# Performance work log

Hardware: AMD Instinct MI355X
Metric: run time of the kernel (lower is better)

The kernel has to match this reference:

```python
import jax, jax.numpy as jnp
import numpy as np

B, L, D = 2, 2048, 1024
H, DH = 16, 64            # heads, dim_head; inner_dim = H*DH = 1024
SCALE = DH ** -0.5


def setup_inputs() -> dict:
    key = jax.random.key(0)
    ks = jax.random.split(key, 7)
    s = 0.02
    return {
        "x": jax.random.normal(ks[0], (B, L, D), dtype=jnp.float32),
        "attention_mask": jnp.zeros((B * H, L, L), dtype=jnp.float32),
        "Wq": jax.random.normal(ks[1], (H * DH, D), dtype=jnp.float32) * s,
        "Wk": jax.random.normal(ks[2], (H * DH, D), dtype=jnp.float32) * s,
        "Wv": jax.random.normal(ks[3], (H * DH, D), dtype=jnp.float32) * s,
        "Wo": jax.random.normal(ks[4], (D, H * DH), dtype=jnp.float32) * s,
        "bo": jnp.zeros((D,), dtype=jnp.float32),
    }


def _split_heads(t):
    # [B, L, H*DH] -> [(B*H), L, DH]
    b, l, _ = t.shape
    return t.reshape(b, l, H, DH).transpose(0, 2, 1, 3).reshape(b * H, l, DH)


def reference(x, attention_mask, Wq, Wk, Wv, Wo, bo):
    # Self-attention: encoder_hidden_states = hidden_states
    q = _split_heads(jnp.einsum('bld,ed->ble', x, Wq))  # [(B*H), L, DH]
    k = _split_heads(jnp.einsum('bld,ed->ble', x, Wk))
    v = _split_heads(jnp.einsum('bld,ed->ble', x, Wv))
    # baddbmm: mask + scale * q @ k^T  -> [(B*H), L, L]
    scores = attention_mask + SCALE * jnp.einsum('nqd,nkd->nqk', q, k)
    probs = jax.nn.softmax(scores, axis=-1)
    hidden = jnp.einsum('nqk,nkd->nqd', probs, v)       # [(B*H), L, DH]
    hidden = hidden.reshape(B, H, L, DH).transpose(0, 2, 1, 3).reshape(B, L, H * DH)
    return jnp.einsum('ble,de->bld', hidden, Wo) + bo   # out projection (dropout=0)
```

## Files before the change

### kernel.cpp

```cpp
#include <hip/hip_runtime.h>


typedef __attribute__((ext_vector_type(8))) short short8;
typedef __attribute__((ext_vector_type(8))) __bf16 bf16x8;
typedef __attribute__((ext_vector_type(4))) float f32x4;

#define GLDS16(gp, lp)                                                         \
  __builtin_amdgcn_global_load_lds(                                            \
      (const __attribute__((address_space(1))) void*)(gp),                     \
      (__attribute__((address_space(3))) void*)(lp), 16, 0, 0)

__device__ __forceinline__ unsigned short f2bf(float f) {
  unsigned u = __builtin_bit_cast(unsigned, f);
  u += 0x7fffu + ((u >> 16) & 1u);
  return (unsigned short)(u >> 16);
}

__global__ __launch_bounds__(256) void convert_all(
    const float* __restrict__ x, const float* __restrict__ wq,
    const float* __restrict__ wk, const float* __restrict__ wv,
    const float* __restrict__ wo, unsigned short* __restrict__ xb,
    unsigned short* __restrict__ wqkv, unsigned short* __restrict__ wob) {
  const int X4 = (2 * 2048 * 1024) / 4;
  const int W4 = (1024 * 1024) / 4;
  const int total = X4 + 4 * W4;
  for (int i = blockIdx.x * 256 + threadIdx.x; i < total;
       i += gridDim.x * 256) {
    const float* src; unsigned short* dst; int off;
    if (i < X4)               { src = x;  dst = xb;                   off = i; }
    else if (i < X4 + W4)     { src = wq; dst = wqkv;                 off = i - X4; }
    else if (i < X4 + 2 * W4) { src = wk; dst = wqkv + 1024 * 1024;   off = i - X4 - W4; }
    else if (i < X4 + 3 * W4) { src = wv; dst = wqkv + 2 * 1024 * 1024; off = i - X4 - 2 * W4; }
    else                      { src = wo; dst = wob;                  off = i - X4 - 3 * W4; }
    float4 v = ((const float4*)src)[off];
    uint2 o;
    o.x = (unsigned)f2bf(v.x) | ((unsigned)f2bf(v.y) << 16);
    o.y = (unsigned)f2bf(v.z) | ((unsigned)f2bf(v.w) << 16);
    ((uint2*)dst)[off] = o;
  }
}

template <int MODE>
__global__ __launch_bounds__(256, 2) void gemm_bt(
    const unsigned short* __restrict__ A, const unsigned short* __restrict__ Bw,
    unsigned short* __restrict__ o_q, unsigned short* __restrict__ o_k,
    unsigned short* __restrict__ o_vT, const float* __restrict__ bias,
    float* __restrict__ o_f) {
  constexpr int K = 1024;
  __shared__ unsigned short As[128 * 32];
  __shared__ unsigned short Bs[128 * 32];
  const int t = threadIdx.x;
  const int w = t >> 6;
  const int lane = t & 63;
  const int g = lane >> 4;
  const int q16 = lane & 15;
  const int wm = w >> 1, wn = w & 1;
  const int bn0 = blockIdx.x * 128, bm0 = blockIdx.y * 128;
  const int arow = t >> 2;
  const int acol = (t & 3) * 8;

  f32x4 acc[4][4];
  const f32x4 z4 = {0.f, 0.f, 0.f, 0.f};
#pragma unroll
  for (int i = 0; i < 4; ++i)
#pragma unroll
    for (int j = 0; j < 4; ++j) acc[i][j] = z4;

  for (int k0 = 0; k0 < K; k0 += 32) {
#pragma unroll
    for (int c = 0; c < 2; ++c) {
      GLDS16(A + (size_t)(bm0 + c * 64 + arow) * K + k0 + acol,
             As + c * 2048 + w * 512);
      GLDS16(Bw + (size_t)(bn0 + c * 64 + arow) * K + k0 + acol,
             Bs + c * 2048 + w * 512);
    }
    __syncthreads();
    bf16x8 af[4], bf[4];
#pragma unroll
    for (int i = 0; i < 4; ++i)
      af[i] = *(const bf16x8*)(As + (wm * 64 + i * 16 + q16) * 32 + g * 8);
#pragma unroll
    for (int j = 0; j < 4; ++j)
      bf[j] = *(const bf16x8*)(Bs + (wn * 64 + j * 16 + q16) * 32 + g * 8);
#pragma unroll
    for (int i = 0; i < 4; ++i)
#pragma unroll
      for (int j = 0; j < 4; ++j)
        acc[i][j] =
            __builtin_amdgcn_mfma_f32_16x16x32_bf16(af[i], bf[j], acc[i][j], 0, 0, 0);
    __syncthreads();
  }

  if constexpr (MODE == 0) {
    const int which = bn0 >> 10;
#pragma unroll
    for (int i = 0; i < 4; ++i)
#pragma unroll
      for (int j = 0; j < 4; ++j)
#pragma unroll
        for (int r = 0; r < 4; ++r) {
          const int m = bm0 + wm * 64 + i * 16 + g * 4 + r;
          const int n = (bn0 & 1023) + wn * 64 + j * 16 + q16;
          const float v = acc[i][j][r];
          const int bb = m >> 11, lp = m & 2047;
          const int h = n >> 6, d = n & 63;
          const int bh = bb * 16 + h;
          if (which == 0)
            o_q[((size_t)bh * 2048 + lp) * 64 + d] = f2bf(v * 0.125f);
          else if (which == 1)
            o_k[((size_t)bh * 2048 + lp) * 64 + d] = f2bf(v);
          else
            o_vT[((size_t)bh * 64 + d) * 2048 + lp] = f2bf(v);
        }
  } else {
#pragma unroll
    for (int i = 0; i < 4; ++i)
#pragma unroll
      for (int j = 0; j < 4; ++j)
#pragma unroll
        for (int r = 0; r < 4; ++r) {
          const int m = bm0 + wm * 64 + i * 16 + g * 4 + r;
          const int n = bn0 + wn * 64 + j * 16 + q16;
          o_f[(size_t)m * 1024 + n] = acc[i][j][r] + bias[n];
        }
  }
}

__global__ __launch_bounds__(256, 3) void attn_kernel(
    const unsigned short* __restrict__ kb, const unsigned short* __restrict__ qb,
    const unsigned short* __restrict__ vT, const float* __restrict__ mask,
    unsigned short* __restrict__ hb) {
  __shared__ float Mst[3 * 2048];
  __shared__ unsigned short Kst[2 * 2048];
  __shared__ unsigned short Vst[2 * 2048];
  __shared__ unsigned short Plds[4][16][40];
  const int orig = blockIdx.x;
  const int bid = (orig & 7) * 128 + (orig >> 3);
  const int bh = bid >> 5, qt = bid & 31;
  const int t = threadIdx.x, w = t >> 6, lane = t & 63;
  const int g = lane >> 4, q16 = lane & 15;
  const int qrow0 = qt * 64;
  const int qrow = qrow0 + w * 16;

  const unsigned short* qptr = qb + ((size_t)bh * 2048 + qrow + q16) * 64 + g * 8;
  bf16x8 qf0 = *(const bf16x8*)(qptr);
  bf16x8 qf1 = *(const bf16x8*)(qptr + 32);

  f32x4 O[4];
  const f32x4 z4 = {0.f, 0.f, 0.f, 0.f};
#pragma unroll
  for (int dt = 0; dt < 4; ++dt) O[dt] = z4;
  float mrun = -1e30f, lsum = 0.f;

  const float* mbase = mask + ((size_t)bh * 2048 + qrow0) * 2048;
  const int fA = (w * 2 + 0) * 64 + lane;
  const int fB = (w * 2 + 1) * 64 + lane;
  const int rA = fA >> 3, cA = (fA & 7) ^ (rA & 7);
  const int rB = fB >> 3, cB = (fB & 7) ^ (rB & 7);
  const float* msrcA = mbase + (size_t)rA * 2048 + cA * 4;
  const float* msrcB = mbase + (size_t)rB * 2048 + cB * 4;
  const int rK = w * 8 + (lane >> 3), cK = (lane & 7) ^ (rK & 7);
  const unsigned short* ksrc = kb + (size_t)bh * 2048 * 64 + (size_t)rK * 64 + cK * 8;
  const int rV = w * 16 + (lane >> 2), cV = (lane & 3) ^ ((rV >> 1) & 3);
  const unsigned short* vsrc = vT + (size_t)bh * 64 * 2048 + (size_t)rV * 2048 + cV * 8;

  const int kx0 = (g ^ (q16 & 7)) * 8;
  const int kx1 = ((g + 4) ^ (q16 & 7)) * 8;
  const int moff0 = (w * 16 + q16) * 32 + (g ^ (q16 & 7)) * 4;
  const int moff1 = (w * 16 + q16) * 32 + ((g + 4) ^ (q16 & 7)) * 4;
  const int vx = (g ^ ((q16 >> 1) & 3)) * 8;

#define STAGE_KV(ti)                                                           \
  do {                                                                         \
    const int kvb_ = ((ti) < 64 ? (ti) : 63) * 32;                             \
    const int b_ = (ti) & 1;                                                   \
    GLDS16(ksrc + (size_t)kvb_ * 64, Kst + b_ * 2048 + w * 512);               \
    GLDS16(vsrc + kvb_, Vst + b_ * 2048 + w * 512);                            \
  } while (0)
#define STAGE_M(ti, b_)                                                        \
  do {                                                                         \
    const int kvb_ = ((ti) < 64 ? (ti) : 63) * 32;                             \
    GLDS16(msrcA + kvb_, Mst + (b_)*2048 + (w * 2 + 0) * 256);                 \
    GLDS16(msrcB + kvb_, Mst + (b_)*2048 + (w * 2 + 1) * 256);                 \
  } while (0)

  STAGE_KV(0);
  STAGE_M(0, 0);
  STAGE_M(1, 1);

  int mb = 0;
  for (int tl = 0; tl < 64; ++tl) {
    asm volatile("s_waitcnt vmcnt(2)" ::: "memory");
    __builtin_amdgcn_s_barrier();
    __builtin_amdgcn_sched_barrier(0);

    STAGE_KV(tl + 1);
    {
      int msb = mb + 2;
      if (msb >= 3) msb -= 3;
      STAGE_M(tl + 2, msb);
    }

    const unsigned short* Kb = Kst + (tl & 1) * 2048;
    const unsigned short* Vb = Vst + (tl & 1) * 2048;
    const float* Mb = Mst + mb * 2048;

    bf16x8 vf[4];
#pragma unroll
    for (int dt = 0; dt < 4; ++dt)
      vf[dt] = *(const bf16x8*)(Vb + (dt * 16 + q16) * 32 + vx);

    bf16x8 kf0 = *(const bf16x8*)(Kb + q16 * 64 + kx0);
    bf16x8 kf1 = *(const bf16x8*)(Kb + q16 * 64 + kx1);
    bf16x8 kf2 = *(const bf16x8*)(Kb + (16 + q16) * 64 + kx0);
    bf16x8 kf3 = *(const bf16x8*)(Kb + (16 + q16) * 64 + kx1);

    f32x4 S0 = z4, S1 = z4;
    S0 = __builtin_amdgcn_mfma_f32_16x16x32_bf16(kf0, qf0, S0, 0, 0, 0);
    S0 = __builtin_amdgcn_mfma_f32_16x16x32_bf16(kf1, qf1, S0, 0, 0, 0);
    S1 = __builtin_amdgcn_mfma_f32_16x16x32_bf16(kf2, qf0, S1, 0, 0, 0);
    S1 = __builtin_amdgcn_mfma_f32_16x16x32_bf16(kf3, qf1, S1, 0, 0, 0);

    S0 += *(const f32x4*)(Mb + moff0);
    S1 += *(const f32x4*)(Mb + moff1);

    float pm = fmaxf(fmaxf(fmaxf(S0[0], S0[1]), fmaxf(S0[2], S0[3])),
                     fmaxf(fmaxf(S1[0], S1[1]), fmaxf(S1[2], S1[3])));
    pm = fmaxf(pm, __shfl_xor(pm, 16));
    pm = fmaxf(pm, __shfl_xor(pm, 32));
    const float mnew = fmaxf(mrun, pm);
    const float alpha = __expf(mrun - mnew);
    float p0[4], p1[4];
    float rs = 0.f;
#pragma unroll
    for (int r = 0; r < 4; ++r) {
      p0[r] = __expf(S0[r] - mnew);
      p1[r] = __expf(S1[r] - mnew);
      rs += p0[r] + p1[r];
    }
    rs += __shfl_xor(rs, 16);
    rs += __shfl_xor(rs, 32);
    lsum = lsum * alpha + rs;
    mrun = mnew;

    float ar[4];
#pragma unroll
    for (int r = 0; r < 4; ++r) ar[r] = __shfl(alpha, g * 4 + r);
#pragma unroll
    for (int dt = 0; dt < 4; ++dt)
#pragma unroll
      for (int r = 0; r < 4; ++r) O[dt][r] *= ar[r];

    uint2 pw0, pw1;
    pw0.x = (unsigned)f2bf(p0[0]) | ((unsigned)f2bf(p0[1]) << 16);
    pw0.y = (unsigned)f2bf(p0[2]) | ((unsigned)f2bf(p0[3]) << 16);
    pw1.x = (unsigned)f2bf(p1[0]) | ((unsigned)f2bf(p1[1]) << 16);
    pw1.y = (unsigned)f2bf(p1[2]) | ((unsigned)f2bf(p1[3]) << 16);
    *(uint2*)&Plds[w][q16][g * 4] = pw0;
    *(uint2*)&Plds[w][q16][16 + g * 4] = pw1;
    bf16x8 pf = *(const bf16x8*)&Plds[w][q16][g * 8];
#pragma unroll
    for (int dt = 0; dt < 4; ++dt)
      O[dt] = __builtin_amdgcn_mfma_f32_16x16x32_bf16(pf, vf[dt], O[dt], 0, 0, 0);

    mb = (mb + 1 >= 3) ? mb + 1 - 3 : mb + 1;
  }
#undef STAGE_KV
#undef STAGE_M

  float li[4];
#pragma unroll
  for (int r = 0; r < 4; ++r) li[r] = 1.f / __shfl(lsum, g * 4 + r);
  const int b = bh >> 4, h = bh & 15;
#pragma unroll
  for (int dt = 0; dt < 4; ++dt)
#pragma unroll
    for (int r = 0; r < 4; ++r) {
      const int qg = qrow + g * 4 + r;
      hb[((size_t)b * 2048 + qg) * 1024 + h * 64 + dt * 16 + q16] =
          f2bf(O[dt][r] * li[r]);
    }
}

extern "C" void kernel_launch(void* const* d_in, const int* in_sizes, int n_in,
                              void* d_out, int out_size, void* d_ws,
                              size_t ws_size, hipStream_t stream) {
  const float* x    = (const float*)d_in[0];
  const float* mask = (const float*)d_in[1];
  const float* wq   = (const float*)d_in[2];
  const float* wk   = (const float*)d_in[3];
  const float* wv   = (const float*)d_in[4];
  const float* wo   = (const float*)d_in[5];
  const float* bo   = (const float*)d_in[6];
  float* out = (float*)d_out;
  char* ws = (char*)d_ws;

  unsigned short* xb   = (unsigned short*)(ws);
  unsigned short* wqkv = (unsigned short*)(ws + 8u * 1024 * 1024);
  unsigned short* wob  = (unsigned short*)(ws + 14u * 1024 * 1024);
  unsigned short* qbuf = (unsigned short*)(ws + 16u * 1024 * 1024);
  unsigned short* kbuf = (unsigned short*)(ws + 24u * 1024 * 1024);
  unsigned short* vTb  = (unsigned short*)(ws + 32u * 1024 * 1024);
  unsigned short* hb   = (unsigned short*)(ws + 40u * 1024 * 1024);
  (void)in_sizes; (void)n_in; (void)out_size; (void)ws_size;

  convert_all<<<2048, 256, 0, stream>>>(x, wq, wk, wv, wo, xb, wqkv, wob);
  gemm_bt<0><<<dim3(24, 32), 256, 0, stream>>>(xb, wqkv, qbuf, kbuf, vTb,
                                               nullptr, nullptr);
  attn_kernel<<<1024, 256, 0, stream>>>(kbuf, qbuf, vTb, mask, hb);
  gemm_bt<1><<<dim3(8, 32), 256, 0, stream>>>(hb, wob, nullptr, nullptr,
                                              nullptr, bo, out);
}
```

Measured before the change: 315.6 us.

## Triple-buffer K/V/mask staging and add lazy softmax rescaling

Stages K and V tiles into a three-deep LDS ring alongside the mask, so all operands are prefetched two tiles ahead under a single unified stage macro. Online softmax now skips the row-max shuffle and the O/lsum rescale unless some value exceeds the running max by more than a threshold of 8. The per-row sum reduction across lanes is deferred to the epilogue. This cuts per-iteration shuffles, exps and rescale multiplies, and hides more load latency. In exchange it uses more LDS, which may lower occupancy, and exp values can grow up to e^8 before bf16 conversion.

```diff
diff --git a/kernel.cpp b/kernel.cpp
--- a/kernel.cpp
+++ b/kernel.cpp
@@ -131,8 +131,8 @@
     const unsigned short* __restrict__ vT, const float* __restrict__ mask,
     unsigned short* __restrict__ hb) {
   __shared__ float Mst[3 * 2048];
-  __shared__ unsigned short Kst[2 * 2048];
-  __shared__ unsigned short Vst[2 * 2048];
+  __shared__ unsigned short Kst[3 * 2048];
+  __shared__ unsigned short Vst[3 * 2048];
   __shared__ unsigned short Plds[4][16][40];
   const int orig = blockIdx.x;
   const int bid = (orig & 7) * 128 + (orig >> 3);
@@ -166,44 +166,33 @@
 
   const int kx0 = (g ^ (q16 & 7)) * 8;
   const int kx1 = ((g + 4) ^ (q16 & 7)) * 8;
-  const int moff0 = (w * 16 + q16) * 32 + (g ^ (q16 & 7)) * 4;
-  const int moff1 = (w * 16 + q16) * 32 + ((g + 4) ^ (q16 & 7)) * 4;
+  const int mo0 = (w * 16 + q16) * 32 + (g ^ (q16 & 7)) * 4;
+  const int mo1 = (w * 16 + q16) * 32 + ((g + 4) ^ (q16 & 7)) * 4;
   const int vx = (g ^ ((q16 >> 1) & 3)) * 8;
 
-#define STAGE_KV(ti)                                                           \
+#define STAGE(ti)                                                              \
   do {                                                                         \
-    const int kvb_ = ((ti) < 64 ? (ti) : 63) * 32;                             \
-    const int b_ = (ti) & 1;                                                   \
-    GLDS16(ksrc + (size_t)kvb_ * 64, Kst + b_ * 2048 + w * 512);               \
-    GLDS16(vsrc + kvb_, Vst + b_ * 2048 + w * 512);                            \
+    const int s_ = (ti) % 3;                                                   \
+    const size_t kvb_ = (size_t)((ti) < 64 ? (ti) : 63) * 32;                  \
+    GLDS16(ksrc + kvb_ * 64, Kst + s_ * 2048 + w * 512);                       \
+    GLDS16(vsrc + kvb_, Vst + s_ * 2048 + w * 512);                            \
+    GLDS16(msrcA + kvb_, Mst + s_ * 2048 + (w * 2 + 0) * 256);                 \
+    GLDS16(msrcB + kvb_, Mst + s_ * 2048 + (w * 2 + 1) * 256);                 \
   } while (0)
-#define STAGE_M(ti, b_)                                                        \
-  do {                                                                         \
-    const int kvb_ = ((ti) < 64 ? (ti) : 63) * 32;                             \
-    GLDS16(msrcA + kvb_, Mst + (b_)*2048 + (w * 2 + 0) * 256);                 \
-    GLDS16(msrcB + kvb_, Mst + (b_)*2048 + (w * 2 + 1) * 256);                 \
-  } while (0)
-
-  STAGE_KV(0);
-  STAGE_M(0, 0);
-  STAGE_M(1, 1);
-
-  int mb = 0;
+
+  STAGE(0);
+  STAGE(1);
   for (int tl = 0; tl < 64; ++tl) {
-    asm volatile("s_waitcnt vmcnt(2)" ::: "memory");
+    asm volatile("s_waitcnt vmcnt(4)" ::: "memory");
     __builtin_amdgcn_s_barrier();
     __builtin_amdgcn_sched_barrier(0);
 
-    STAGE_KV(tl + 1);
-    {
-      int msb = mb + 2;
-      if (msb >= 3) msb -= 3;
-      STAGE_M(tl + 2, msb);
-    }
-
-    const unsigned short* Kb = Kst + (tl & 1) * 2048;
-    const unsigned short* Vb = Vst + (tl & 1) * 2048;
-    const float* Mb = Mst + mb * 2048;
+    STAGE(tl + 2);
+
+    const int sb = tl % 3;
+    const unsigned short* Kb = Kst + sb * 2048;
+    const unsigned short* Vb = Vst + sb * 2048;
+    const float* Mb = Mst + sb * 2048;
 
     bf16x8 vf[4];
 #pragma unroll
@@ -221,35 +210,35 @@
     S1 = __builtin_amdgcn_mfma_f32_16x16x32_bf16(kf2, qf0, S1, 0, 0, 0);
     S1 = __builtin_amdgcn_mfma_f32_16x16x32_bf16(kf3, qf1, S1, 0, 0, 0);
 
-    S0 += *(const f32x4*)(Mb + moff0);
-    S1 += *(const f32x4*)(Mb + moff1);
-
-    float pm = fmaxf(fmaxf(fmaxf(S0[0], S0[1]), fmaxf(S0[2], S0[3])),
-                     fmaxf(fmaxf(S1[0], S1[1]), fmaxf(S1[2], S1[3])));
-    pm = fmaxf(pm, __shfl_xor(pm, 16));
-    pm = fmaxf(pm, __shfl_xor(pm, 32));
-    const float mnew = fmaxf(mrun, pm);
-    const float alpha = __expf(mrun - mnew);
-    float p0[4], p1[4];
-    float rs = 0.f;
+    S0 += *(const f32x4*)(Mb + mo0);
+    S1 += *(const f32x4*)(Mb + mo1);
+
+    float lmax = fmaxf(fmaxf(fmaxf(S0[0], S0[1]), fmaxf(S0[2], S0[3])),
+                       fmaxf(fmaxf(S1[0], S1[1]), fmaxf(S1[2], S1[3])));
+    if (!__all(lmax <= mrun + 8.f)) {
+      float pm = fmaxf(lmax, __shfl_xor(lmax, 16));
+      pm = fmaxf(pm, __shfl_xor(pm, 32));
+      const float mnew = fmaxf(mrun, pm);
+      const float alpha = __expf(mrun - mnew);
+      lsum *= alpha;
+      float ar[4];
+#pragma unroll
+      for (int r = 0; r < 4; ++r) ar[r] = __shfl(alpha, g * 4 + r);
+#pragma unroll
+      for (int dt = 0; dt < 4; ++dt)
+#pragma unroll
+        for (int r = 0; r < 4; ++r) O[dt][r] *= ar[r];
+      mrun = mnew;
+    }
+
+    float p0[4], p1[4], rs = 0.f;
 #pragma unroll
     for (int r = 0; r < 4; ++r) {
-      p0[r] = __expf(S0[r] - mnew);
-      p1[r] = __expf(S1[r] - mnew);
+      p0[r] = __expf(S0[r] - mrun);
+      p1[r] = __expf(S1[r] - mrun);
       rs += p0[r] + p1[r];
     }
-    rs += __shfl_xor(rs, 16);
-    rs += __shfl_xor(rs, 32);
-    lsum = lsum * alpha + rs;
-    mrun = mnew;
-
-    float ar[4];
-#pragma unroll
-    for (int r = 0; r < 4; ++r) ar[r] = __shfl(alpha, g * 4 + r);
-#pragma unroll
-    for (int dt = 0; dt < 4; ++dt)
-#pragma unroll
-      for (int r = 0; r < 4; ++r) O[dt][r] *= ar[r];
+    lsum += rs;
 
     uint2 pw0, pw1;
     pw0.x = (unsigned)f2bf(p0[0]) | ((unsigned)f2bf(p0[1]) << 16);
@@ -262,15 +251,14 @@
 #pragma unroll
     for (int dt = 0; dt < 4; ++dt)
       O[dt] = __builtin_amdgcn_mfma_f32_16x16x32_bf16(pf, vf[dt], O[dt], 0, 0, 0);
-
-    mb = (mb + 1 >= 3) ? mb + 1 - 3 : mb + 1;
   }
-#undef STAGE_KV
-#undef STAGE_M
-
+#undef STAGE
+
+  float rsrow = lsum + __shfl_xor(lsum, 16);
+  rsrow += __shfl_xor(rsrow, 32);
   float li[4];
 #pragma unroll
-  for (int r = 0; r < 4; ++r) li[r] = 1.f / __shfl(lsum, g * 4 + r);
+  for (int r = 0; r < 4; ++r) li[r] = 1.f / __shfl(rsrow, g * 4 + r);
   const int b = bh >> 4, h = bh & 15;
 #pragma unroll
   for (int dt = 0; dt < 4; ++dt)
```

Measured after the change: 299.7 us. 1.05x faster.
